# Kernel optimization log

Hardware: AMD Instinct MI355X
Metric: run time of the kernel (lower is better)

The kernel has to match this reference:

```python
import jax, jax.numpy as jnp
import numpy as np

B, N, C = 32, 262144, 5
ALPHA = 50.0
EPS_LS = 0.2
BASE_W = [0.8, 2.0, 1.5, 1.5, 3.5]
# (cid, ref, sign): height_diff = sign*(pr_z[cid] - gt_z[ref]); violation = sigmoid(-10*diff)
# Enumerates all z_above / z_below pairs in the hierarchy dict.
PAIRS = [(1, 2, -1.0), (1, 3, -1.0), (1, 4, -1.0),
         (2, 1, 1.0), (2, 3, -1.0), (2, 4, -1.0),
         (3, 1, 1.0), (3, 2, 1.0), (3, 4, -1.0),
         (4, 1, 1.0), (4, 2, 1.0), (4, 3, 1.0)]


def setup_inputs() -> dict:
    key = jax.random.key(0)
    k1, k2, k3 = jax.random.split(key, 3)
    outputs = jax.random.normal(k1, (B, C, N), dtype=jnp.float32)
    labels = jax.random.randint(k2, (B, N), 0, C, dtype=jnp.int32)
    points = jax.random.normal(k3, (B, N, 3), dtype=jnp.float32)
    return {"outputs": outputs, "labels": labels, "points": points}


def _centroid(points, mask):
    # points: [B,N,3], mask: [B,N] bool -> ([B,3], [B] valid)
    valid = mask.any(axis=1)
    m = mask.astype(points.dtype)
    s = jnp.einsum('bn,bnd->bd', m, points)
    cnt = jnp.clip(m.sum(axis=1), 1.0)
    return s / cnt[:, None], valid


def _forward(outputs, points, labels):
    logits = jnp.transpose(outputs, (0, 2, 1))  # [B,N,C]
    b = labels.shape[0]
    preds = jnp.argmax(logits, axis=-1)  # [B,N]
    base = jnp.asarray(BASE_W, dtype=logits.dtype)
    weights = jnp.broadcast_to(base, (b, C))
    gt_c = {cid: _centroid(points, labels == cid) for cid in (1, 2, 3, 4)}
    pr_c = {cid: _centroid(points, preds == cid) for cid in (1, 2, 3, 4)}
    # hierarchy violation scatter into per-batch class weights
    for cid, ref, sign in PAIRS:
        pr_pos, pos_valid = pr_c[cid]
        gt_ref, ref_valid = gt_c[ref]
        valid = ref_valid & pos_valid
        diff = sign * (pr_pos[:, 2] - gt_ref[:, 2])
        add = jnp.where(valid, ALPHA * jax.nn.sigmoid(-diff * 10.0), 0.0)
        weights = weights.at[:, cid].add(add).at[:, ref].add(0.3 * add)
    # predicted bounding boxes of masked points (zeros included, as in torch)
    bounds = {}
    for cid in (2, 3):
        mp = points * (preds == cid)[:, :, None].astype(points.dtype)
        bounds[cid] = jnp.stack([mp.min(axis=1), mp.max(axis=1)], axis=1)  # [B,2,3]
    for cid in (2, 3):
        rb = bounds[3 if cid == 2 else 2]
        xc = (bounds[cid][:, :, 0] - rb[:, 0:1, 0]) / (rb[:, 1:2, 0] - rb[:, 0:1, 0] + 1e-7)
        yc = (bounds[cid][:, :, 1] - rb[:, 0:1, 1]) / (rb[:, 1:2, 1] - rb[:, 0:1, 1] + 1e-7)
        viol = ((xc < 0.1) | (xc > 0.9)) | ((yc < 0.1) | (yc > 0.9))
        weights = weights.at[:, cid].add(ALPHA * viol.astype(weights.dtype).mean(axis=1))
    weights = jnp.clip(weights, 0.1, 10.0)
    # inverse-sqrt class frequency weights
    dist = jnp.bincount(labels.reshape(-1), length=C).astype(logits.dtype)
    cw = 1.0 / (jnp.sqrt(dist) + 1e-7)
    cw = cw / cw.sum() * C
    w = weights.mean(axis=0) * cw  # [C]
    # weighted cross entropy with label_smoothing=0.2 (PyTorch semantics)
    logp = jax.nn.log_softmax(logits.reshape(-1, C), axis=-1)
    y = labels.reshape(-1)
    wt = w[y]
    wsum = wt.sum()
    nll = (wt * -jnp.take_along_axis(logp, y[:, None], axis=1)[:, 0]).sum() / wsum
    smooth = (-(logp * w[None, :]).sum(axis=-1)).sum() / wsum
    return (1.0 - EPS_LS) * nll + (EPS_LS / C) * smooth


def reference(outputs, labels, points):
    return _forward(outputs, points, labels)
```

## Files before the change

### kernel.cpp

```cpp
#include <hip/hip_runtime.h>
#include <math.h>

#define NPTS 262144
#define BATCH 32
#define NCLS 5

__device__ __forceinline__ float wred_sum(float v) {
#pragma unroll
    for (int o = 32; o; o >>= 1) v += __shfl_down(v, o);
    return v;
}
__device__ __forceinline__ unsigned wred_usum(unsigned v) {
#pragma unroll
    for (int o = 32; o; o >>= 1) v += __shfl_down(v, o);
    return v;
}
__device__ __forceinline__ float wred_min(float v) {
#pragma unroll
    for (int o = 32; o; o >>= 1) v = fminf(v, __shfl_down(v, o));
    return v;
}
__device__ __forceinline__ float wred_max(float v) {
#pragma unroll
    for (int o = 32; o; o >>= 1) v = fmaxf(v, __shfl_down(v, o));
    return v;
}


__global__ __launch_bounds__(256) void bsl_main(
    const float* __restrict__ outputs, const int* __restrict__ labels,
    const float* __restrict__ points, float* __restrict__ pf,
    unsigned int* __restrict__ pi, int bpb, int iters)
{
    const int blk = blockIdx.x;
    const int nblk = gridDim.x;
    const int b = blk / bpb;
    const int seg = blk % bpb;
    const int seg_start = seg * (iters * 1024);
    const int tid = threadIdx.x;

    float S[5] = {0, 0, 0, 0, 0};
    float T[5] = {0, 0, 0, 0, 0};
    float lseacc = 0.f;
    float gtz[4] = {0, 0, 0, 0};
    float prz[4] = {0, 0, 0, 0};
    const float INF = __int_as_float(0x7f800000);
    float mn2x = INF, mx2x = -INF, mn2y = INF, mx2y = -INF;
    float mn3x = INF, mx3x = -INF, mn3y = INF, mx3y = -INF;
    unsigned bc[5] = {0, 0, 0, 0, 0}, gtc[4] = {0, 0, 0, 0}, prc[4] = {0, 0, 0, 0};

    const float* obase = outputs + (size_t)b * NCLS * NPTS;
    const int*   lbase = labels + (size_t)b * NPTS;
    const float* pbase = points + (size_t)b * NPTS * 3;

    for (int it = 0; it < iters; ++it) {
        const int n = seg_start + it * 1024 + tid * 4;
        float4 L[5];
#pragma unroll
        for (int c = 0; c < 5; ++c)
            L[c] = *(const float4*)(obase + (size_t)c * NPTS + n);
        const int4 lab = *(const int4*)(lbase + n);
        const float4* pp = (const float4*)(pbase + (size_t)n * 3);
        const float4 p0 = pp[0], p1 = pp[1], p2 = pp[2];
        const float xs[4] = {p0.x, p0.w, p1.z, p2.y};
        const float ys[4] = {p0.y, p1.x, p1.w, p2.z};
        const float zs[4] = {p0.z, p1.y, p2.x, p2.w};
        const int   lb[4] = {lab.x, lab.y, lab.z, lab.w};
#pragma unroll
        for (int j = 0; j < 4; ++j) {
            float v[5];
#pragma unroll
            for (int c = 0; c < 5; ++c) v[c] = ((const float*)&L[c])[j];
            float best = v[0]; int pred = 0;
#pragma unroll
            for (int c = 1; c < 5; ++c)
                if (v[c] > best) { best = v[c]; pred = c; }
            float e = 0.f;
#pragma unroll
            for (int c = 0; c < 5; ++c) e += __expf(v[c] - best);
            const float lse = best + __logf(e);
            lseacc += lse;
            const int y = lb[j];
#pragma unroll
            for (int c = 0; c < 5; ++c) {
                S[c] += v[c];
                const bool is = (y == c);
                T[c] += is ? (lse - v[c]) : 0.f;
                bc[c] += is ? 1u : 0u;
            }
            const float z = zs[j];
#pragma unroll
            for (int k = 0; k < 4; ++k) {
                const bool gy = (y == k + 1), py = (pred == k + 1);
                gtz[k] += gy ? z : 0.f; gtc[k] += gy ? 1u : 0u;
                prz[k] += py ? z : 0.f; prc[k] += py ? 1u : 0u;
            }
            const float x = xs[j], yv = ys[j];
            const float a2x = (pred == 2) ? x : 0.f;
            const float a2y = (pred == 2) ? yv : 0.f;
            const float a3x = (pred == 3) ? x : 0.f;
            const float a3y = (pred == 3) ? yv : 0.f;
            mn2x = fminf(mn2x, a2x); mx2x = fmaxf(mx2x, a2x);
            mn2y = fminf(mn2y, a2y); mx2y = fmaxf(mx2y, a2y);
            mn3x = fminf(mn3x, a3x); mx3x = fmaxf(mx3x, a3x);
            mn3y = fminf(mn3y, a3y); mx3y = fmaxf(mx3y, a3y);
        }
    }

    float fv[27] = {S[0], S[1], S[2], S[3], S[4],
                    T[0], T[1], T[2], T[3], T[4],
                    lseacc,
                    gtz[0], gtz[1], gtz[2], gtz[3],
                    prz[0], prz[1], prz[2], prz[3],
                    mn2x, mx2x, mn2y, mx2y, mn3x, mx3x, mn3y, mx3y};
    unsigned iv[13] = {bc[0], bc[1], bc[2], bc[3], bc[4],
                       gtc[0], gtc[1], gtc[2], gtc[3],
                       prc[0], prc[1], prc[2], prc[3]};

    __shared__ float sf[4][27];
    __shared__ unsigned si[4][13];
    const int wid = tid >> 6, lane = tid & 63;
#pragma unroll
    for (int vdx = 0; vdx < 27; ++vdx) {
        float r;
        if (vdx < 19) r = wred_sum(fv[vdx]);
        else if (((vdx - 19) & 1) == 0) r = wred_min(fv[vdx]);
        else r = wred_max(fv[vdx]);
        if (lane == 0) sf[wid][vdx] = r;
    }
#pragma unroll
    for (int vdx = 0; vdx < 13; ++vdx) {
        unsigned r = wred_usum(iv[vdx]);
        if (lane == 0) si[wid][vdx] = r;
    }
    __syncthreads();
    if (tid == 0) {
#pragma unroll
        for (int vdx = 0; vdx < 27; ++vdx) {
            float r;
            if (vdx < 19) r = sf[0][vdx] + sf[1][vdx] + sf[2][vdx] + sf[3][vdx];
            else if (((vdx - 19) & 1) == 0)
                r = fminf(fminf(sf[0][vdx], sf[1][vdx]), fminf(sf[2][vdx], sf[3][vdx]));
            else
                r = fmaxf(fmaxf(sf[0][vdx], sf[1][vdx]), fmaxf(sf[2][vdx], sf[3][vdx]));
            pf[(size_t)vdx * nblk + blk] = r;
        }
#pragma unroll
        for (int vdx = 0; vdx < 13; ++vdx)
            pi[(size_t)vdx * nblk + blk] = si[0][vdx] + si[1][vdx] + si[2][vdx] + si[3][vdx];
    }
}

__global__ __launch_bounds__(64) void bsl_reduce(
    const float* __restrict__ pf, const unsigned int* __restrict__ pi,
    int bpb, float* __restrict__ s2)
{
    const int nblk = BATCH * bpb;
    const int t = blockIdx.x;
    const int lane = threadIdx.x;
    const float INF = __int_as_float(0x7f800000);
    if (t < 11) {
        const float4* p4 = (const float4*)(pf + (size_t)t * nblk);
        const int n4 = nblk >> 2;
        float s = 0.f;
#pragma unroll 8
        for (int i = lane; i < n4; i += 64) {
            const float4 v = p4[i];
            s += (v.x + v.y) + (v.z + v.w);
        }
        s = wred_sum(s);
        if (lane == 0) s2[t] = s;
    } else if (t < 16) {
        const int v = t - 11;
        const uint4* p4 = (const uint4*)(pi + (size_t)v * nblk);
        const int n4 = nblk >> 2;
        unsigned s = 0;
#pragma unroll 8
        for (int i = lane; i < n4; i += 64) {
            const uint4 u = p4[i];
            s += u.x + u.y + u.z + u.w;
        }
        s = wred_usum(s);
        if (lane == 0) s2[t] = (float)s;
    } else {
        const int u = t - 16;
        const int b = u / 24;
        const int f = u % 24;
        const int base = b * bpb;
        if (f < 8) {
            float s = 0.f;
            for (int i = lane; i < bpb; i += 64) s += pf[(size_t)(11 + f) * nblk + base + i];
            s = wred_sum(s);
            if (lane == 0) s2[t] = s;
        } else if (f < 16) {
            const int g = f - 8;
            const bool ismin = ((g & 1) == 0);
            float s = ismin ? INF : -INF;
            for (int i = lane; i < bpb; i += 64) {
                const float x = pf[(size_t)(19 + g) * nblk + base + i];
                s = ismin ? fminf(s, x) : fmaxf(s, x);
            }
            s = ismin ? wred_min(s) : wred_max(s);
            if (lane == 0) s2[t] = s;
        } else {
            const int g = f - 16;
            unsigned s = 0;
            for (int i = lane; i < bpb; i += 64) s += pi[(size_t)(5 + g) * nblk + base + i];
            s = wred_usum(s);
            if (lane == 0) s2[t] = (float)s;
        }
    }
}

__global__ __launch_bounds__(64) void bsl_final(
    const float* __restrict__ s2, float* __restrict__ out)
{
    __shared__ float sm[16 + 24 * BATCH];
    const int lane = threadIdx.x;
    for (int i = lane; i < 16 + 24 * BATCH; i += 64) sm[i] = s2[i];
    __syncthreads();

    const float BASE_W[5] = {0.8f, 2.0f, 1.5f, 1.5f, 3.5f};
    const int pc[12]  = {1, 1, 1, 2, 2, 2, 3, 3, 3, 4, 4, 4};
    const int prf[12] = {2, 3, 4, 1, 3, 4, 1, 2, 4, 1, 2, 3};
    const float ps[12] = {-1.f, -1.f, -1.f, 1.f, -1.f, -1.f, 1.f, 1.f, -1.f, 1.f, 1.f, 1.f};

    float w[5] = {0, 0, 0, 0, 0};
    if (lane < BATCH) {
        const float* R = sm + 16 + lane * 24;
        for (int c = 0; c < 5; ++c) w[c] = BASE_W[c];
        float gtm[4], prm[4];
        bool gv[4], pv[4];
#pragma unroll
        for (int k = 0; k < 4; ++k) {
            const float c1 = R[16 + k];
            gv[k] = (c1 > 0.f);
            gtm[k] = R[k] / fmaxf(c1, 1.f);
            const float c2 = R[20 + k];
            pv[k] = (c2 > 0.f);
            prm[k] = R[4 + k] / fmaxf(c2, 1.f);
        }
#pragma unroll
        for (int p = 0; p < 12; ++p) {
            const int cid = pc[p], ref = prf[p];
            float add = 0.f;
            if (pv[cid - 1] && gv[ref - 1]) {
                const float diff = ps[p] * (prm[cid - 1] - gtm[ref - 1]);
                add = 50.f / (1.f + expf(10.f * diff));
            }
            w[cid] += add;
            w[ref] += 0.3f * add;
        }
        const float mn2x = R[8],  mx2x = R[9],  mn2y = R[10], mx2y = R[11];
        const float mn3x = R[12], mx3x = R[13], mn3y = R[14], mx3y = R[15];
        {
            const float dx = mx3x - mn3x + 1e-7f, dy = mx3y - mn3y + 1e-7f;
            const float xc0 = (mn2x - mn3x) / dx, xc1 = (mx2x - mn3x) / dx;
            const float yc0 = (mn2y - mn3y) / dy, yc1 = (mx2y - mn3y) / dy;
            const float v0 = (xc0 < 0.1f || xc0 > 0.9f || yc0 < 0.1f || yc0 > 0.9f) ? 1.f : 0.f;
            const float v1 = (xc1 < 0.1f || xc1 > 0.9f || yc1 < 0.1f || yc1 > 0.9f) ? 1.f : 0.f;
            w[2] += 50.f * 0.5f * (v0 + v1);
        }
        {
            const float dx = mx2x - mn2x + 1e-7f, dy = mx2y - mn2y + 1e-7f;
            const float xc0 = (mn3x - mn2x) / dx, xc1 = (mx3x - mn2x) / dx;
            const float yc0 = (mn3y - mn2y) / dy, yc1 = (mx3y - mn2y) / dy;
            const float v0 = (xc0 < 0.1f || xc0 > 0.9f || yc0 < 0.1f || yc0 > 0.9f) ? 1.f : 0.f;
            const float v1 = (xc1 < 0.1f || xc1 > 0.9f || yc1 < 0.1f || yc1 > 0.9f) ? 1.f : 0.f;
            w[3] += 50.f * 0.5f * (v0 + v1);
        }
#pragma unroll
        for (int c = 0; c < 5; ++c)
            w[c] = fminf(fmaxf(w[c], 0.1f), 10.f);
    }
    float wsumc[5];
#pragma unroll
    for (int c = 0; c < 5; ++c) wsumc[c] = wred_sum(w[c]);

    if (lane == 0) {
        float dist[5], cw[5], s = 0.f;
#pragma unroll
        for (int c = 0; c < 5; ++c) {
            dist[c] = sm[11 + c];
            cw[c] = 1.f / (sqrtf(dist[c]) + 1e-7f);
            s += cw[c];
        }
        float wf[5], wsum = 0.f, W = 0.f, nllnum = 0.f, Ssum = 0.f;
#pragma unroll
        for (int c = 0; c < 5; ++c) {
            cw[c] = cw[c] / s * 5.f;
            wf[c] = (wsumc[c] / 32.f) * cw[c];
            wsum += wf[c] * dist[c];
            W += wf[c];
            nllnum += wf[c] * sm[5 + c];
            Ssum += wf[c] * sm[c];
        }
        const float nll = nllnum / wsum;
        const float smooth = (W * sm[10] - Ssum) / wsum;
        out[0] = 0.8f * nll + 0.04f * smooth;
    }
}

extern "C" void kernel_launch(void* const* d_in, const int* in_sizes, int n_in,
                              void* d_out, int out_size, void* d_ws, size_t ws_size,
                              hipStream_t stream) {
    const float* outputs = (const float*)d_in[0];
    const int*   labels  = (const int*)d_in[1];
    const float* points  = (const float*)d_in[2];
    float* out = (float*)d_out;

    const size_t S2N = 16 + 24 * BATCH;
    int bpb = 64;
    while (bpb > 1 &&
           (size_t)(27 + 13) * 4 * BATCH * (size_t)bpb + S2N * 4 > ws_size)
        bpb >>= 1;
    const int nblk = BATCH * bpb;
    const int iters = NPTS / (bpb * 1024);

    float* pf = (float*)d_ws;
    unsigned int* pi = (unsigned int*)(pf + (size_t)27 * nblk);
    float* s2 = (float*)(pi + (size_t)13 * nblk);

    bsl_main<<<nblk, 256, 0, stream>>>(outputs, labels, points, pf, pi, bpb, iters);
    bsl_reduce<<<(int)S2N, 64, 0, stream>>>(pf, pi, bpb, s2);
    bsl_final<<<1, 64, 0, stream>>>(s2, out);
}
```

Before: 72.01 us.

## Raise grid size, template iteration count, fuse final kernel via last-block counter

Blocks per batch go from 64 to 256, so each block handles one 1024-point chunk and the iteration count becomes a template parameter with a fully unrolled loop. The final scalar kernel is folded into the reduce kernel using an atomic counter, where the last block computes the loss, which removes one launch. Ground-truth class counts are no longer accumulated separately; they are taken from the existing label bincount rows. The cost is four times as many per-block partials to reduce, plus reliance on the counter reset done by block 0 of the main kernel.

Result: slower. 117.9 us (+63.8%).

```diff
diff --git a/kernel.cpp b/kernel.cpp
--- a/kernel.cpp
+++ b/kernel.cpp
@@ -3,7 +3,6 @@
 
 #define NPTS 262144
 #define BATCH 32
-#define NCLS 5
 
 __device__ __forceinline__ float wred_sum(float v) {
 #pragma unroll
@@ -27,17 +26,20 @@
 }
 
 
+template<int ITERS>
 __global__ __launch_bounds__(256) void bsl_main(
     const float* __restrict__ outputs, const int* __restrict__ labels,
     const float* __restrict__ points, float* __restrict__ pf,
-    unsigned int* __restrict__ pi, int bpb, int iters)
+    unsigned int* __restrict__ pi, int bpb, unsigned int* __restrict__ counter)
 {
     const int blk = blockIdx.x;
     const int nblk = gridDim.x;
     const int b = blk / bpb;
     const int seg = blk % bpb;
-    const int seg_start = seg * (iters * 1024);
+    const int seg_start = seg * (ITERS * 1024);
     const int tid = threadIdx.x;
+
+    if (blk == 0 && tid == 0) *counter = 0u;
 
     float S[5] = {0, 0, 0, 0, 0};
     float T[5] = {0, 0, 0, 0, 0};
@@ -47,13 +49,14 @@
     const float INF = __int_as_float(0x7f800000);
     float mn2x = INF, mx2x = -INF, mn2y = INF, mx2y = -INF;
     float mn3x = INF, mx3x = -INF, mn3y = INF, mx3y = -INF;
-    unsigned bc[5] = {0, 0, 0, 0, 0}, gtc[4] = {0, 0, 0, 0}, prc[4] = {0, 0, 0, 0};
-
-    const float* obase = outputs + (size_t)b * NCLS * NPTS;
+    unsigned bc[5] = {0, 0, 0, 0, 0}, prc[4] = {0, 0, 0, 0};
+
+    const float* obase = outputs + (size_t)b * 5 * NPTS;
     const int*   lbase = labels + (size_t)b * NPTS;
     const float* pbase = points + (size_t)b * NPTS * 3;
 
-    for (int it = 0; it < iters; ++it) {
+#pragma unroll
+    for (int it = 0; it < ITERS; ++it) {
         const int n = seg_start + it * 1024 + tid * 4;
         float4 L[5];
 #pragma unroll
@@ -92,8 +95,9 @@
 #pragma unroll
             for (int k = 0; k < 4; ++k) {
                 const bool gy = (y == k + 1), py = (pred == k + 1);
-                gtz[k] += gy ? z : 0.f; gtc[k] += gy ? 1u : 0u;
-                prz[k] += py ? z : 0.f; prc[k] += py ? 1u : 0u;
+                gtz[k] += gy ? z : 0.f;
+                prz[k] += py ? z : 0.f;
+                prc[k] += py ? 1u : 0u;
             }
             const float x = xs[j], yv = ys[j];
             const float a2x = (pred == 2) ? x : 0.f;
@@ -113,12 +117,11 @@
                     gtz[0], gtz[1], gtz[2], gtz[3],
                     prz[0], prz[1], prz[2], prz[3],
                     mn2x, mx2x, mn2y, mx2y, mn3x, mx3x, mn3y, mx3y};
-    unsigned iv[13] = {bc[0], bc[1], bc[2], bc[3], bc[4],
-                       gtc[0], gtc[1], gtc[2], gtc[3],
-                       prc[0], prc[1], prc[2], prc[3]};
+    unsigned iv[9] = {bc[0], bc[1], bc[2], bc[3], bc[4],
+                      prc[0], prc[1], prc[2], prc[3]};
 
     __shared__ float sf[4][27];
-    __shared__ unsigned si[4][13];
+    __shared__ unsigned si[4][9];
     const int wid = tid >> 6, lane = tid & 63;
 #pragma unroll
     for (int vdx = 0; vdx < 27; ++vdx) {
@@ -129,7 +132,7 @@
         if (lane == 0) sf[wid][vdx] = r;
     }
 #pragma unroll
-    for (int vdx = 0; vdx < 13; ++vdx) {
+    for (int vdx = 0; vdx < 9; ++vdx) {
         unsigned r = wred_usum(iv[vdx]);
         if (lane == 0) si[wid][vdx] = r;
     }
@@ -146,19 +149,23 @@
             pf[(size_t)vdx * nblk + blk] = r;
         }
 #pragma unroll
-        for (int vdx = 0; vdx < 13; ++vdx)
+        for (int vdx = 0; vdx < 9; ++vdx)
             pi[(size_t)vdx * nblk + blk] = si[0][vdx] + si[1][vdx] + si[2][vdx] + si[3][vdx];
     }
 }
 
 __global__ __launch_bounds__(64) void bsl_reduce(
     const float* __restrict__ pf, const unsigned int* __restrict__ pi,
-    int bpb, float* __restrict__ s2)
+    int bpb, float* __restrict__ s2, unsigned int* __restrict__ counter,
+    float* __restrict__ out)
 {
     const int nblk = BATCH * bpb;
     const int t = blockIdx.x;
     const int lane = threadIdx.x;
     const float INF = __int_as_float(0x7f800000);
+    __shared__ int isLast;
+    __shared__ float sm[16 + 24 * BATCH];
+
     if (t < 11) {
         const float4* p4 = (const float4*)(pf + (size_t)t * nblk);
         const int n4 = nblk >> 2;
@@ -204,19 +211,23 @@
             if (lane == 0) s2[t] = s;
         } else {
             const int g = f - 16;
+            const int row = (g < 4) ? (1 + g) : (5 + (g - 4));
             unsigned s = 0;
-            for (int i = lane; i < bpb; i += 64) s += pi[(size_t)(5 + g) * nblk + base + i];
+            for (int i = lane; i < bpb; i += 64) s += pi[(size_t)row * nblk + base + i];
             s = wred_usum(s);
             if (lane == 0) s2[t] = (float)s;
         }
     }
-}
-
-__global__ __launch_bounds__(64) void bsl_final(
-    const float* __restrict__ s2, float* __restrict__ out)
-{
-    __shared__ float sm[16 + 24 * BATCH];
-    const int lane = threadIdx.x;
+
+    if (lane == 0) {
+        __threadfence();
+        const unsigned old = atomicAdd(counter, 1u);
+        isLast = (old == (unsigned)(gridDim.x - 1)) ? 1 : 0;
+    }
+    __syncthreads();
+    if (!isLast) return;
+    __threadfence();
+
     for (int i = lane; i < 16 + 24 * BATCH; i += 64) sm[i] = s2[i];
     __syncthreads();
 
@@ -310,18 +321,24 @@
     float* out = (float*)d_out;
 
     const size_t S2N = 16 + 24 * BATCH;
-    int bpb = 64;
+    int bpb = 256;
     while (bpb > 1 &&
-           (size_t)(27 + 13) * 4 * BATCH * (size_t)bpb + S2N * 4 > ws_size)
+           (size_t)(27 + 9) * 4 * BATCH * (size_t)bpb + S2N * 4 + 4 > ws_size)
         bpb >>= 1;
     const int nblk = BATCH * bpb;
-    const int iters = NPTS / (bpb * 1024);
+    const int iters = 256 / bpb;
 
     float* pf = (float*)d_ws;
     unsigned int* pi = (unsigned int*)(pf + (size_t)27 * nblk);
-    float* s2 = (float*)(pi + (size_t)13 * nblk);
-
-    bsl_main<<<nblk, 256, 0, stream>>>(outputs, labels, points, pf, pi, bpb, iters);
-    bsl_reduce<<<(int)S2N, 64, 0, stream>>>(pf, pi, bpb, s2);
-    bsl_final<<<1, 64, 0, stream>>>(s2, out);
-}
+    float* s2 = (float*)(pi + (size_t)9 * nblk);
+    unsigned int* counter = (unsigned int*)(s2 + S2N);
+
+    switch (iters) {
+        case 1:  bsl_main<1><<<nblk, 256, 0, stream>>>(outputs, labels, points, pf, pi, bpb, counter); break;
+        case 2:  bsl_main<2><<<nblk, 256, 0, stream>>>(outputs, labels, points, pf, pi, bpb, counter); break;
+        case 4:  bsl_main<4><<<nblk, 256, 0, stream>>>(outputs, labels, points, pf, pi, bpb, counter); break;
+        case 8:  bsl_main<8><<<nblk, 256, 0, stream>>>(outputs, labels, points, pf, pi, bpb, counter); break;
+        default: bsl_main<16><<<nblk, 256, 0, stream>>>(outputs, labels, points, pf, pi, bpb, counter); break;
+    }
+    bsl_reduce<<<(int)S2N, 64, 0, stream>>>(pf, pi, bpb, s2, counter, out);
+}
```
